# Performance work log

Measured on AMD Instinct MI355X. Metric: run time of the kernel, lower is better.

The kernel has to match this reference:

```python
import jax, jax.numpy as jnp
import numpy as np

N_DATES, M_ASSETS, N_SIMS = 64, 64, 32768


def setup_inputs() -> dict:
    key = jax.random.key(0)
    k1, k2, k3 = jax.random.split(key, 3)
    cov = jax.random.normal(k1, (N_DATES, M_ASSETS, M_ASSETS), dtype=jnp.float32)
    var = jax.random.uniform(k2, (N_DATES, M_ASSETS, 1), dtype=jnp.float32)
    z = jax.random.normal(k3, (N_DATES, M_ASSETS, N_SIMS), dtype=jnp.float32)
    return {"cov": cov, "var": var, "z": z}


def reference(cov, var, z):
    # Per-date increment: dW[i] = cov[i] @ z[i] - var[i]/2, shapes [n,m,S]
    dW = jnp.einsum('nij,njs->nis', cov, z) - var * 0.5
    # logsamples at date i is the running sum of increments (parallel scan)
    logsamples = jnp.cumsum(dW, axis=0)  # [n, m, S]
    return logsamples
```

## Files before the change

kernel.cpp:

```cpp
#include <hip/hip_runtime.h>

#define NDATES 64
#define MASSETS 64
#define NSIMS 32768
#define SB 64

typedef __attribute__((ext_vector_type(8))) short bf16x8;
typedef __attribute__((ext_vector_type(4))) float f32x4;

__device__ __forceinline__ unsigned short f2bf(float f) {
    union { float f; unsigned u; } c; c.f = f;
    unsigned x = c.u;
    x += 0x7FFFu + ((x >> 16) & 1u);
    return (unsigned short)(x >> 16);
}

__global__ __launch_bounds__(256) void evo_lognormal_kernel(
    const float* __restrict__ cov,
    const float* __restrict__ var,
    const float* __restrict__ z,
    float* __restrict__ out)
{
    __shared__ __align__(16) unsigned short zs[SB * 64];

    const int t    = threadIdx.x;
    const int wv   = t >> 6;
    const int lane = t & 63;
    const int Q    = lane >> 2;
    const int q    = lane & 3;
    const int l15  = lane & 15;
    const int lg   = lane >> 4;
    const int s0   = blockIdx.x * SB;

    f32x4 acc[4];
    #pragma unroll
    for (int i = 0; i < 4; ++i) acc[i] = f32x4{0.f, 0.f, 0.f, 0.f};
    float vs0 = 0.f, vs1 = 0.f, vs2 = 0.f, vs3 = 0.f;

    const int arow = wv * 16 + l15;
    const int r0   = wv * 16 + (lg << 2);

    for (int d = 0; d < NDATES; ++d) {
        const float* zd = z + ((size_t)d << 21) + s0;

        __syncthreads();

        #pragma unroll
        for (int it = 0; it < 4; ++it) {
            const int kb = it * 16 + wv * 4;
            const float4 v4 = *reinterpret_cast<const float4*>(
                zd + (size_t)(kb + q) * NSIMS + 4 * Q);
            float v0 = v4.x, v1 = v4.y, v2 = v4.z, v3 = v4.w;
            float s01 = __shfl_xor(v1, 1), s10 = __shfl_xor(v0, 1);
            float s23 = __shfl_xor(v3, 1), s32 = __shfl_xor(v2, 1);
            float a0 = (q & 1) ? s01 : v0;
            float a1 = (q & 1) ? v1  : s10;
            float a2 = (q & 1) ? s23 : v2;
            float a3 = (q & 1) ? v3  : s32;
            float u02 = __shfl_xor(a2, 2), u20 = __shfl_xor(a0, 2);
            float u13 = __shfl_xor(a3, 2), u31 = __shfl_xor(a1, 2);
            float w0 = (q & 2) ? u02 : a0;
            float w1 = (q & 2) ? u13 : a1;
            float w2 = (q & 2) ? a2  : u20;
            float w3 = (q & 2) ? a3  : u31;
            const int sh = 4 * Q + q;
            unsigned lo = (unsigned)f2bf(w0) | ((unsigned)f2bf(w1) << 16);
            unsigned hi = (unsigned)f2bf(w2) | ((unsigned)f2bf(w3) << 16);
            const int u = sh * 64 + (kb ^ ((sh & 7) << 3));
            *reinterpret_cast<uint2*>(&zs[u]) = make_uint2(lo, hi);
        }

        const float* cbase = cov + (((size_t)d * 64 + arow) << 6) + (lg << 3);
        const float4 c0 = *reinterpret_cast<const float4*>(cbase);
        const float4 c1 = *reinterpret_cast<const float4*>(cbase + 4);
        const float4 c2 = *reinterpret_cast<const float4*>(cbase + 32);
        const float4 c3 = *reinterpret_cast<const float4*>(cbase + 36);
        bf16x8 afr0, afr1;
        afr0[0] = (short)f2bf(c0.x); afr0[1] = (short)f2bf(c0.y);
        afr0[2] = (short)f2bf(c0.z); afr0[3] = (short)f2bf(c0.w);
        afr0[4] = (short)f2bf(c1.x); afr0[5] = (short)f2bf(c1.y);
        afr0[6] = (short)f2bf(c1.z); afr0[7] = (short)f2bf(c1.w);
        afr1[0] = (short)f2bf(c2.x); afr1[1] = (short)f2bf(c2.y);
        afr1[2] = (short)f2bf(c2.z); afr1[3] = (short)f2bf(c2.w);
        afr1[4] = (short)f2bf(c3.x); afr1[5] = (short)f2bf(c3.y);
        afr1[6] = (short)f2bf(c3.z); afr1[7] = (short)f2bf(c3.w);

        __syncthreads();

        #pragma unroll
        for (int ct = 0; ct < 4; ++ct) {
            const int sl = ct * 16 + l15;
            const int u0 = sl * 64 + ((lg << 3) ^ ((l15 & 7) << 3));
            bf16x8 b0 = *reinterpret_cast<const bf16x8*>(&zs[u0]);
            bf16x8 b1 = *reinterpret_cast<const bf16x8*>(&zs[u0 ^ 32]);
            acc[ct] = __builtin_amdgcn_mfma_f32_16x16x32_bf16(afr0, b0, acc[ct], 0, 0, 0);
            acc[ct] = __builtin_amdgcn_mfma_f32_16x16x32_bf16(afr1, b1, acc[ct], 0, 0, 0);
        }

        const float* vp = var + d * 64 + r0;
        vs0 += 0.5f * vp[0];
        vs1 += 0.5f * vp[1];
        vs2 += 0.5f * vp[2];
        vs3 += 0.5f * vp[3];

        float* ob = out + (((size_t)d * 64 + r0) << 15) + s0 + l15;
        #pragma unroll
        for (int ct = 0; ct < 4; ++ct) {
            ob[ct * 16]                = acc[ct][0] - vs0;
            ob[(1 << 15) + ct * 16]    = acc[ct][1] - vs1;
            ob[(2 << 15) + ct * 16]    = acc[ct][2] - vs2;
            ob[(3 << 15) + ct * 16]    = acc[ct][3] - vs3;
        }
    }
}

extern "C" void kernel_launch(void* const* d_in, const int* in_sizes, int n_in,
                              void* d_out, int out_size, void* d_ws, size_t ws_size,
                              hipStream_t stream) {
    const float* cov = (const float*)d_in[0];
    const float* var = (const float*)d_in[1];
    const float* z   = (const float*)d_in[2];
    float* out = (float*)d_out;
    dim3 grid(NSIMS / SB);
    dim3 block(256);
    evo_lognormal_kernel<<<grid, block, 0, stream>>>(cov, var, z, out);
}
```

Before: 224.6 us.

## Prefetch next z tile into registers, precast cov to bf16, swap MFMA operands

Adds a small pre-kernel that converts cov to bf16 in workspace, so the main kernel stops converting it every date in every block. Swaps MFMA operand roles so z comes from LDS as the A operand and cov is read directly from global as B. The output is then laid out so each lane stores a float4 along the sims dimension. The next date's z tile is loaded into registers before the current MFMA, overlapping global latency with compute, at the cost of more registers, a second launch and the workspace.

```diff
diff --git a/kernel.cpp b/kernel.cpp
--- a/kernel.cpp
+++ b/kernel.cpp
@@ -15,8 +15,18 @@
     return (unsigned short)(x >> 16);
 }
 
+__global__ __launch_bounds__(256) void cov_prep_kernel(
+    const float* __restrict__ cov, unsigned short* __restrict__ cw)
+{
+    const int i = (blockIdx.x * 256 + threadIdx.x) * 4;
+    const float4 v = *reinterpret_cast<const float4*>(cov + i);
+    ushort4 o;
+    o.x = f2bf(v.x); o.y = f2bf(v.y); o.z = f2bf(v.z); o.w = f2bf(v.w);
+    *reinterpret_cast<ushort4*>(cw + i) = o;
+}
+
 __global__ __launch_bounds__(256) void evo_lognormal_kernel(
-    const float* __restrict__ cov,
+    const unsigned short* __restrict__ cw,
     const float* __restrict__ var,
     const float* __restrict__ z,
     float* __restrict__ out)
@@ -35,22 +45,28 @@
     f32x4 acc[4];
     #pragma unroll
     for (int i = 0; i < 4; ++i) acc[i] = f32x4{0.f, 0.f, 0.f, 0.f};
-    float vs0 = 0.f, vs1 = 0.f, vs2 = 0.f, vs3 = 0.f;
+    float vs[4] = {0.f, 0.f, 0.f, 0.f};
 
-    const int arow = wv * 16 + l15;
-    const int r0   = wv * 16 + (lg << 2);
+    const int srow = wv * 16 + l15;
+    const int ard  = srow * 64 + ((lg << 3) ^ ((l15 & 7) << 3));
+
+    float4 zr[4];
+    const float* zb = z + s0;
+    {
+        #pragma unroll
+        for (int it = 0; it < 4; ++it) {
+            const int kb = it * 16 + wv * 4;
+            zr[it] = *reinterpret_cast<const float4*>(zb + (size_t)(kb + q) * NSIMS + 4 * Q);
+        }
+    }
 
     for (int d = 0; d < NDATES; ++d) {
-        const float* zd = z + ((size_t)d << 21) + s0;
-
-        __syncthreads();
+        if (d) __syncthreads();
 
         #pragma unroll
         for (int it = 0; it < 4; ++it) {
             const int kb = it * 16 + wv * 4;
-            const float4 v4 = *reinterpret_cast<const float4*>(
-                zd + (size_t)(kb + q) * NSIMS + 4 * Q);
-            float v0 = v4.x, v1 = v4.y, v2 = v4.z, v3 = v4.w;
+            float v0 = zr[it].x, v1 = zr[it].y, v2 = zr[it].z, v3 = zr[it].w;
             float s01 = __shfl_xor(v1, 1), s10 = __shfl_xor(v0, 1);
             float s23 = __shfl_xor(v3, 1), s32 = __shfl_xor(v2, 1);
             float a0 = (q & 1) ? s01 : v0;
@@ -70,46 +86,42 @@
             *reinterpret_cast<uint2*>(&zs[u]) = make_uint2(lo, hi);
         }
 
-        const float* cbase = cov + (((size_t)d * 64 + arow) << 6) + (lg << 3);
-        const float4 c0 = *reinterpret_cast<const float4*>(cbase);
-        const float4 c1 = *reinterpret_cast<const float4*>(cbase + 4);
-        const float4 c2 = *reinterpret_cast<const float4*>(cbase + 32);
-        const float4 c3 = *reinterpret_cast<const float4*>(cbase + 36);
-        bf16x8 afr0, afr1;
-        afr0[0] = (short)f2bf(c0.x); afr0[1] = (short)f2bf(c0.y);
-        afr0[2] = (short)f2bf(c0.z); afr0[3] = (short)f2bf(c0.w);
-        afr0[4] = (short)f2bf(c1.x); afr0[5] = (short)f2bf(c1.y);
-        afr0[6] = (short)f2bf(c1.z); afr0[7] = (short)f2bf(c1.w);
-        afr1[0] = (short)f2bf(c2.x); afr1[1] = (short)f2bf(c2.y);
-        afr1[2] = (short)f2bf(c2.z); afr1[3] = (short)f2bf(c2.w);
-        afr1[4] = (short)f2bf(c3.x); afr1[5] = (short)f2bf(c3.y);
-        afr1[6] = (short)f2bf(c3.z); afr1[7] = (short)f2bf(c3.w);
-
         __syncthreads();
 
+        if (d + 1 < NDATES) {
+            const float* zd = zb + ((size_t)(d + 1) << 21);
+            #pragma unroll
+            for (int it = 0; it < 4; ++it) {
+                const int kb = it * 16 + wv * 4;
+                zr[it] = *reinterpret_cast<const float4*>(zd + (size_t)(kb + q) * NSIMS + 4 * Q);
+            }
+        }
+
+        bf16x8 a0 = *reinterpret_cast<const bf16x8*>(&zs[ard]);
+        bf16x8 a1 = *reinterpret_cast<const bf16x8*>(&zs[ard ^ 32]);
+
+        const unsigned short* cb = cw + (((d << 6) + l15) << 6) + (lg << 3);
         #pragma unroll
         for (int ct = 0; ct < 4; ++ct) {
-            const int sl = ct * 16 + l15;
-            const int u0 = sl * 64 + ((lg << 3) ^ ((l15 & 7) << 3));
-            bf16x8 b0 = *reinterpret_cast<const bf16x8*>(&zs[u0]);
-            bf16x8 b1 = *reinterpret_cast<const bf16x8*>(&zs[u0 ^ 32]);
-            acc[ct] = __builtin_amdgcn_mfma_f32_16x16x32_bf16(afr0, b0, acc[ct], 0, 0, 0);
-            acc[ct] = __builtin_amdgcn_mfma_f32_16x16x32_bf16(afr1, b1, acc[ct], 0, 0, 0);
+            bf16x8 b0 = *reinterpret_cast<const bf16x8*>(cb + (ct << 10));
+            bf16x8 b1 = *reinterpret_cast<const bf16x8*>(cb + (ct << 10) + 32);
+            acc[ct] = __builtin_amdgcn_mfma_f32_16x16x32_bf16(a0, b0, acc[ct], 0, 0, 0);
+            acc[ct] = __builtin_amdgcn_mfma_f32_16x16x32_bf16(a1, b1, acc[ct], 0, 0, 0);
         }
 
-        const float* vp = var + d * 64 + r0;
-        vs0 += 0.5f * vp[0];
-        vs1 += 0.5f * vp[1];
-        vs2 += 0.5f * vp[2];
-        vs3 += 0.5f * vp[3];
+        const float* vp = var + (d << 6) + l15;
+        #pragma unroll
+        for (int ct = 0; ct < 4; ++ct) vs[ct] += 0.5f * vp[ct << 4];
 
-        float* ob = out + (((size_t)d * 64 + r0) << 15) + s0 + l15;
+        float* ob = out + (((size_t)d << 21)) + s0 + wv * 16 + (lg << 2);
         #pragma unroll
         for (int ct = 0; ct < 4; ++ct) {
-            ob[ct * 16]                = acc[ct][0] - vs0;
-            ob[(1 << 15) + ct * 16]    = acc[ct][1] - vs1;
-            ob[(2 << 15) + ct * 16]    = acc[ct][2] - vs2;
-            ob[(3 << 15) + ct * 16]    = acc[ct][3] - vs3;
+            float4 o;
+            o.x = acc[ct][0] - vs[ct];
+            o.y = acc[ct][1] - vs[ct];
+            o.z = acc[ct][2] - vs[ct];
+            o.w = acc[ct][3] - vs[ct];
+            *reinterpret_cast<float4*>(ob + ((size_t)(ct * 16 + l15) << 15)) = o;
         }
     }
 }
@@ -121,7 +133,8 @@
     const float* var = (const float*)d_in[1];
     const float* z   = (const float*)d_in[2];
     float* out = (float*)d_out;
-    dim3 grid(NSIMS / SB);
-    dim3 block(256);
-    evo_lognormal_kernel<<<grid, block, 0, stream>>>(cov, var, z, out);
+    unsigned short* cw = (unsigned short*)d_ws;
+
+    cov_prep_kernel<<<dim3(NDATES * MASSETS * MASSETS / 1024), dim3(256), 0, stream>>>(cov, cw);
+    evo_lognormal_kernel<<<dim3(NSIMS / SB), dim3(256), 0, stream>>>(cw, var, z, out);
 }
```

Result: slower. 309.9 us (+37.9%).
